# Optimization experiments

Hardware: AMD Instinct MI355X
Metric: run time of the kernel (lower is better)

Reference implementation:

```python
import jax, jax.numpy as jnp
import numpy as np

B = 100_000   # graph nodes in batch
C = 1_000     # virtual-node clusters
D = 512       # in_dim (attention hidden dim)
OUT = 512     # out_dim


def setup_inputs() -> dict:
    key = jax.random.key(0)
    ks = jax.random.split(key, 9)
    h = jax.random.normal(ks[0], (B, D), dtype=jnp.float32)
    g = jax.random.normal(ks[1], (C, D), dtype=jnp.float32)
    # vn_index[:,1] is the cluster id of node i; arange%C guarantees every
    # cluster is present, so the per-cluster concat has exactly C rows in
    # sorted-cluster-id order (matching torch .unique() iteration order).
    vn_index = jnp.stack([jnp.arange(B, dtype=jnp.int32),
                          jnp.arange(B, dtype=jnp.int32) % C], axis=1)
    n_id = jnp.arange(B, dtype=jnp.int32)
    s = 1.0 / np.sqrt(D)
    Wq = jax.random.uniform(ks[2], (D, D), jnp.float32, -s, s)   # query_proj (no bias)
    Wk = jax.random.uniform(ks[3], (D, D), jnp.float32, -s, s)   # key_proj (no bias)
    attn_bias = jax.random.uniform(ks[4], (D,), jnp.float32, -0.1, 0.1)
    Ws = jax.random.uniform(ks[5], (1, D), jnp.float32, -s, s)   # score_proj weight
    bs = jax.random.uniform(ks[6], (1,), jnp.float32, -s, s)     # score_proj bias
    so = 1.0 / np.sqrt(D)
    W = jax.random.uniform(ks[7], (OUT, D), jnp.float32, -so, so)  # final Linear
    b = jax.random.uniform(ks[8], (OUT,), jnp.float32, -so, so)
    return {"h": h, "g": g, "vn_index": vn_index, "n_id": n_id,
            "Wq": Wq, "Wk": Wk, "attn_bias": attn_bias, "Ws": Ws, "bs": bs,
            "W": W, "b": b}


def reference(h, g, vn_index, n_id, Wq, Wk, attn_bias, Ws, bs, W, b):
    # cluster id for each batch node (B,)
    cluster = vn_index[n_id, 1]
    # additive attention, vectorized over all nodes (replaces per-cluster loop)
    qp = g @ Wq.T                                   # (C, D) query proj per cluster
    kp = h @ Wk.T                                   # (B, D) key proj per node
    score = jnp.tanh(kp + qp[cluster] + attn_bias) @ Ws[0] + bs[0]  # (B,)
    # segment softmax over each cluster
    smax = jax.ops.segment_max(score, cluster, num_segments=C)      # (C,)
    e = jnp.exp(score - smax[cluster])                              # (B,)
    denom = jax.ops.segment_sum(e, cluster, num_segments=C)         # (C,)
    attn = e / denom[cluster]                                       # (B,)
    # attention-weighted sum of node features per cluster -> (C, D)
    ctx = jax.ops.segment_sum(attn[:, None] * h, cluster, num_segments=C)
    # final projection + tanh activation -> (C, OUT)
    return jnp.tanh(ctx @ W.T + b)
```

## Files before the change

kernel.cpp:

```cpp
#include <hip/hip_runtime.h>
#include <stdint.h>

#define D_DIM 512

typedef __attribute__((ext_vector_type(8))) short bf16x8;
typedef __attribute__((ext_vector_type(4))) float f32x4;
typedef __attribute__((ext_vector_type(4))) short short4_t;
typedef __attribute__((ext_vector_type(4))) float float4_t;

__device__ __forceinline__ unsigned short f2bf(float f) {
  unsigned u = __float_as_uint(f);
  u += 0x7FFFu + ((u >> 16) & 1u);
  return (unsigned short)(u >> 16);
}

__device__ __forceinline__ float bf2f(unsigned short s) {
  return __uint_as_float(((unsigned)s) << 16);
}

__device__ __forceinline__ float tanh_fast(float x) {
  float e = __expf(2.0f * x);
  return 1.0f - 2.0f / (e + 1.0f);
}

#define GLOAD_LDS16(gsrc, ldst) \
  __builtin_amdgcn_global_load_lds((const __attribute__((address_space(1))) void*)(gsrc), \
                                   (__attribute__((address_space(3))) void*)(ldst), 16, 0, 0)


__global__ void cvt_f32_bf16_k(const float* __restrict__ in, unsigned short* __restrict__ out, int n4) {
  int i = blockIdx.x * blockDim.x + threadIdx.x;
  if (i < n4) {
    float4_t v = ((const float4_t*)in)[i];
    short4_t s;
    s.x = (short)f2bf(v.x); s.y = (short)f2bf(v.y);
    s.z = (short)f2bf(v.z); s.w = (short)f2bf(v.w);
    ((short4_t*)out)[i] = s;
  }
}

__global__ void cvt3_f32_bf16_k(const float* __restrict__ a, const float* __restrict__ b,
                                const float* __restrict__ c, unsigned short* __restrict__ out,
                                int n4each) {
  int i = blockIdx.x * blockDim.x + threadIdx.x;
  if (i >= 3 * n4each) return;
  int sel = i / n4each, j = i - sel * n4each;
  const float* src = (sel == 0) ? a : (sel == 1) ? b : c;
  float4_t v = ((const float4_t*)src)[j];
  short4_t s;
  s.x = (short)f2bf(v.x); s.y = (short)f2bf(v.y);
  s.z = (short)f2bf(v.z); s.w = (short)f2bf(v.w);
  ((short4_t*)out)[i] = s;
}

__global__ void prep_cluster_k(const int* __restrict__ vn, const int* __restrict__ nid,
                               int* __restrict__ cl, int* __restrict__ counts, int B) {
  int i = blockIdx.x * blockDim.x + threadIdx.x;
  if (i < B) {
    int c = vn[2 * nid[i] + 1];
    cl[i] = c;
    atomicAdd(&counts[c], 1);
  }
}

__global__ void prefix_k(const int* __restrict__ counts, int* __restrict__ starts,
                         int* __restrict__ cursor, int C) {
  __shared__ int sh[1024];
  int t = threadIdx.x;
  int v = (t < C) ? counts[t] : 0;
  sh[t] = v;
  __syncthreads();
  for (int off = 1; off < 1024; off <<= 1) {
    int x = (t >= off) ? sh[t - off] : 0;
    __syncthreads();
    sh[t] += x;
    __syncthreads();
  }
  if (t < C) { int st = sh[t] - v; starts[t] = st; cursor[t] = st; }
  if (t == 1023) starts[C] = sh[1023];
}

__global__ void scatter_k(const int* __restrict__ cl, int* __restrict__ cursor,
                          int* __restrict__ order, int B) {
  int i = blockIdx.x * blockDim.x + threadIdx.x;
  if (i < B) {
    int pos = atomicAdd(&cursor[cl[i]], 1);
    order[pos] = i;
  }
}

__device__ __forceinline__ unsigned enc_f(float f) {
  unsigned u = __float_as_uint(f);
  return (u & 0x80000000u) ? ~u : (u | 0x80000000u);
}
__device__ __forceinline__ float dec_f(unsigned u) {
  return __uint_as_float((u & 0x80000000u) ? (u & 0x7FFFFFFFu) : ~u);
}

__global__ void seg_max_k(const float* __restrict__ score, const int* __restrict__ cl,
                          unsigned* __restrict__ smax, int B) {
  int i = blockIdx.x * blockDim.x + threadIdx.x;
  if (i < B) atomicMax(&smax[cl[i]], enc_f(score[i]));
}

__global__ void seg_expsum_k(const float* __restrict__ score, const int* __restrict__ cl,
                             const unsigned* __restrict__ smax, float* __restrict__ ev,
                             float* __restrict__ denom, int B) {
  int i = blockIdx.x * blockDim.x + threadIdx.x;
  if (i < B) {
    int c = cl[i];
    float x = __expf(score[i] - dec_f(smax[c]));
    ev[i] = x;
    atomicAdd(&denom[c], x);
  }
}

__global__ __launch_bounds__(256)
void ctx_k(const unsigned short* __restrict__ hbf, const float* __restrict__ ev,
           const int* __restrict__ order, const int* __restrict__ starts,
           const float* __restrict__ denom, float* __restrict__ ctx) {
  int c = blockIdx.x;
  int t = threadIdx.x;
  int s0 = starts[c], s1 = starts[c + 1];
  float a0 = 0.f, a1 = 0.f;
  int j = s0;
  for (; j + 3 < s1; j += 4) {
    int i0 = order[j], i1 = order[j + 1], i2 = order[j + 2], i3 = order[j + 3];
    float e0 = ev[i0], e1 = ev[i1], e2 = ev[i2], e3 = ev[i3];
    unsigned u0 = *(const unsigned*)(hbf + (size_t)i0 * D_DIM + t * 2);
    unsigned u1 = *(const unsigned*)(hbf + (size_t)i1 * D_DIM + t * 2);
    unsigned u2 = *(const unsigned*)(hbf + (size_t)i2 * D_DIM + t * 2);
    unsigned u3 = *(const unsigned*)(hbf + (size_t)i3 * D_DIM + t * 2);
    a0 += e0 * bf2f((unsigned short)u0) + e1 * bf2f((unsigned short)u1)
        + e2 * bf2f((unsigned short)u2) + e3 * bf2f((unsigned short)u3);
    a1 += e0 * bf2f((unsigned short)(u0 >> 16)) + e1 * bf2f((unsigned short)(u1 >> 16))
        + e2 * bf2f((unsigned short)(u2 >> 16)) + e3 * bf2f((unsigned short)(u3 >> 16));
  }
  for (; j < s1; ++j) {
    int i0 = order[j];
    float e0 = ev[i0];
    unsigned u0 = *(const unsigned*)(hbf + (size_t)i0 * D_DIM + t * 2);
    a0 += e0 * bf2f((unsigned short)u0);
    a1 += e0 * bf2f((unsigned short)(u0 >> 16));
  }
  float inv = 1.0f / denom[c];
  float2 r = make_float2(a0 * inv, a1 * inv);
  *(float2*)(&ctx[(size_t)c * D_DIM + t * 2]) = r;
}

__global__ __launch_bounds__(1024)
void gemm256sq_score_k(const unsigned short* __restrict__ Abf,
                       const unsigned short* __restrict__ Bw, int M,
                       const float* __restrict__ qb, const int* __restrict__ cl,
                       const float* __restrict__ Ws, float* __restrict__ out)
{
  __shared__ unsigned short AB[2][16384];
  __shared__ float red[256][4];
  __shared__ int clds[256];

  const int t = threadIdx.x;
  const int lane = t & 63;
  const int w = t >> 6;
  const int wr = w >> 2, wc = w & 3;
  const int l15 = lane & 15, l4 = lane >> 4;

  int id;
  {
    int nwg = gridDim.x;
    int q = nwg >> 3, r = nwg & 7;
    int xcd = blockIdx.x & 7, pos = blockIdx.x >> 3;
    id = (xcd < r ? xcd * (q + 1) : r * (q + 1) + (xcd - r) * q) + pos;
  }
  const int n0 = (id & 1) * 256;
  const int m0 = (id >> 1) * 256;

  const int rin = lane >> 2;
  const int lrow = w * 16 + rin;
  const int sslot = (lane & 3) ^ ((lrow >> 1) & 3);
  int rowA = m0 + lrow; if (rowA > M - 1) rowA = M - 1;
  const unsigned short* srcA = Abf + (size_t)rowA * 512 + sslot * 8;
  const unsigned short* srcB = Bw + (size_t)(n0 + lrow) * 512 + sslot * 8;

  int offA[4], offB[4];
  #pragma unroll
  for (int mi = 0; mi < 4; ++mi) {
    int row = wr * 64 + mi * 16 + l15;
    offA[mi] = row * 64 + ((l4 ^ ((row >> 1) & 3)) * 16);
  }
  #pragma unroll
  for (int ni = 0; ni < 4; ++ni) {
    int row = wc * 64 + ni * 16 + l15;
    offB[ni] = 16384 + row * 64 + ((l4 ^ ((row >> 1) & 3)) * 16);
  }

  f32x4 acc[4][4];
  #pragma unroll
  for (int mi = 0; mi < 4; ++mi)
    #pragma unroll
    for (int ni = 0; ni < 4; ++ni)
      acc[mi][ni] = (f32x4){0.f, 0.f, 0.f, 0.f};

  GLOAD_LDS16(srcA, ((char*)&AB[0][0]) + w * 1024);
  GLOAD_LDS16(srcB, ((char*)&AB[0][8192]) + w * 1024);
  __builtin_amdgcn_sched_barrier(0);

  #pragma unroll
  for (int kt = 0; kt < 16; ++kt) {
    const int b = kt & 1;
    asm volatile("s_waitcnt vmcnt(0)" ::: "memory");
    __builtin_amdgcn_sched_barrier(0);
    __builtin_amdgcn_s_barrier();
    __builtin_amdgcn_sched_barrier(0);

    if (kt < 15) {
      const int k1 = (kt + 1) * 32;
      GLOAD_LDS16(srcA + k1, ((char*)&AB[b ^ 1][0]) + w * 1024);
      GLOAD_LDS16(srcB + k1, ((char*)&AB[b ^ 1][8192]) + w * 1024);
    }

    bf16x8 a[4], bv[4];
    #pragma unroll
    for (int mi = 0; mi < 4; ++mi)
      a[mi] = *(const bf16x8*)(((const char*)AB[b]) + offA[mi]);
    #pragma unroll
    for (int ni = 0; ni < 4; ++ni)
      bv[ni] = *(const bf16x8*)(((const char*)AB[b]) + offB[ni]);
    __builtin_amdgcn_s_setprio(1);
    #pragma unroll
    for (int mi = 0; mi < 4; ++mi)
      #pragma unroll
      for (int ni = 0; ni < 4; ++ni)
        acc[mi][ni] = __builtin_amdgcn_mfma_f32_16x16x32_bf16(a[mi], bv[ni], acc[mi][ni], 0, 0, 0);
    __builtin_amdgcn_s_setprio(0);
    __builtin_amdgcn_sched_barrier(0);
  }

  if (t < 256) {
    int gm = m0 + t;
    clds[t] = cl[gm < M ? gm : M - 1];
  }
  __syncthreads();
  #pragma unroll
  for (int mi = 0; mi < 4; ++mi) {
    #pragma unroll
    for (int r = 0; r < 4; ++r) {
      int rowt = wr * 64 + mi * 16 + l4 * 4 + r;
      int c = clds[rowt];
      const float* qrow = &qb[(size_t)c * 512];
      float s = 0.f;
      #pragma unroll
      for (int ni = 0; ni < 4; ++ni) {
        int gcol = n0 + wc * 64 + ni * 16 + l15;
        float x = acc[mi][ni][r] + qrow[gcol];
        s += tanh_fast(x) * Ws[gcol];
      }
      s += __shfl_xor(s, 1);
      s += __shfl_xor(s, 2);
      s += __shfl_xor(s, 4);
      s += __shfl_xor(s, 8);
      if (l15 == 0) red[rowt][wc] = s;
    }
  }
  __syncthreads();
  if (t < 256) {
    int gm = m0 + t;
    if (gm < M) atomicAdd(&out[gm], red[t][0] + red[t][1] + red[t][2] + red[t][3]);
  }
}

template<int EPI>
__global__ __launch_bounds__(256)
void gemm128_k(const unsigned short* __restrict__ Abf,
               const unsigned short* __restrict__ Bw, int M,
               const float* __restrict__ bias, float* __restrict__ out)
{
  __shared__ unsigned short As[2][128 * 32];
  __shared__ unsigned short Bs[2][128 * 32];

  const int t = threadIdx.x;
  const int lane = t & 63;
  const int w = t >> 6;
  const int wr = w >> 1, wc = w & 1;
  const int l15 = lane & 15, l4 = lane >> 4;

  const int nwg = gridDim.x;
  int id = blockIdx.x;
  if ((nwg & 7) == 0) id = (id & 7) * (nwg >> 3) + (id >> 3);
  const int n0 = (id & 3) * 128;
  const int m0 = (id >> 2) * 128;

  const int rin = lane >> 2;
  const int sl = lane & 3;

  const unsigned short* srcA[2];
  const unsigned short* srcB[2];
  int dstOff[2];
  #pragma unroll
  for (int c = 0; c < 2; ++c) {
    int chunk = w * 2 + c;
    int row = chunk * 16 + rin;
    int slot = sl ^ ((row >> 1) & 3);
    int ga = m0 + row; if (ga > M - 1) ga = M - 1;
    srcA[c] = Abf + (size_t)ga * 512 + slot * 8;
    srcB[c] = Bw + (size_t)(n0 + row) * 512 + slot * 8;
    dstOff[c] = chunk * 1024;
  }

  int offA[4], offB[4];
  #pragma unroll
  for (int mi = 0; mi < 4; ++mi) {
    int row = wr * 64 + mi * 16 + l15;
    offA[mi] = row * 64 + ((l4 ^ ((row >> 1) & 3)) * 16);
  }
  #pragma unroll
  for (int ni = 0; ni < 4; ++ni) {
    int row = wc * 64 + ni * 16 + l15;
    offB[ni] = row * 64 + ((l4 ^ ((row >> 1) & 3)) * 16);
  }

  f32x4 acc[4][4];
  #pragma unroll
  for (int mi = 0; mi < 4; ++mi)
    #pragma unroll
    for (int ni = 0; ni < 4; ++ni)
      acc[mi][ni] = (f32x4){0.f, 0.f, 0.f, 0.f};

  #pragma unroll
  for (int c = 0; c < 2; ++c) {
    GLOAD_LDS16(srcA[c], ((char*)As[0]) + dstOff[c]);
    GLOAD_LDS16(srcB[c], ((char*)Bs[0]) + dstOff[c]);
  }
  __builtin_amdgcn_sched_barrier(0);

  #pragma unroll
  for (int it = 0; it < 16; ++it) {
    const int cur = it & 1;
    asm volatile("s_waitcnt vmcnt(0)" ::: "memory");
    __builtin_amdgcn_sched_barrier(0);
    __builtin_amdgcn_s_barrier();
    __builtin_amdgcn_sched_barrier(0);
    if (it < 15) {
      const int k1 = (it + 1) * 32;
      #pragma unroll
      for (int c = 0; c < 2; ++c) {
        GLOAD_LDS16(srcA[c] + k1, ((char*)As[cur ^ 1]) + dstOff[c]);
        GLOAD_LDS16(srcB[c] + k1, ((char*)Bs[cur ^ 1]) + dstOff[c]);
      }
    }
    {
      bf16x8 af[4], bfv[4];
      #pragma unroll
      for (int mi = 0; mi < 4; ++mi)
        af[mi] = *(const bf16x8*)(((const char*)As[cur]) + offA[mi]);
      #pragma unroll
      for (int ni = 0; ni < 4; ++ni)
        bfv[ni] = *(const bf16x8*)(((const char*)Bs[cur]) + offB[ni]);
      #pragma unroll
      for (int mi = 0; mi < 4; ++mi)
        #pragma unroll
        for (int ni = 0; ni < 4; ++ni)
          acc[mi][ni] = __builtin_amdgcn_mfma_f32_16x16x32_bf16(af[mi], bfv[ni], acc[mi][ni], 0, 0, 0);
    }
    __builtin_amdgcn_sched_barrier(0);
  }

  #pragma unroll
  for (int mi = 0; mi < 4; ++mi) {
    #pragma unroll
    for (int r = 0; r < 4; ++r) {
      int gm = m0 + wr * 64 + mi * 16 + l4 * 4 + r;
      if (gm < M) {
        #pragma unroll
        for (int ni = 0; ni < 4; ++ni) {
          int gcol = n0 + wc * 64 + ni * 16 + l15;
          float v = acc[mi][ni][r] + bias[gcol];
          if (EPI == 2) v = tanh_fast(v);
          out[(size_t)gm * 512 + gcol] = v;
        }
      }
    }
  }
}


extern "C" void kernel_launch(void* const* d_in, const int* in_sizes, int n_in,
                              void* d_out, int out_size, void* d_ws, size_t ws_size,
                              hipStream_t stream) {
  const float* h  = (const float*)d_in[0];
  const float* g  = (const float*)d_in[1];
  const int*   vn = (const int*)d_in[2];
  const int*   nid= (const int*)d_in[3];
  const float* Wq = (const float*)d_in[4];
  const float* Wk = (const float*)d_in[5];
  const float* ab = (const float*)d_in[6];
  const float* Ws = (const float*)d_in[7];
  const float* W  = (const float*)d_in[9];
  const float* b  = (const float*)d_in[10];

  const int B = in_sizes[3];
  const int C = in_sizes[1] / D_DIM;

  char* wsb = (char*)d_ws;
  size_t off = 0;
  auto alloc = [&](size_t bytes) -> void* {
    void* p = wsb + off;
    off += (bytes + 255) & ~(size_t)255;
    return p;
  };

  unsigned short* hbf   = (unsigned short*)alloc((size_t)B * 512 * 2);
  unsigned short* gbf   = (unsigned short*)alloc((size_t)C * 512 * 2);
  unsigned short* ctxbf = (unsigned short*)alloc((size_t)C * 512 * 2);
  unsigned short* Wk_bf = (unsigned short*)alloc((size_t)512 * 512 * 2);
  unsigned short* Wq_bf = (unsigned short*)alloc((size_t)512 * 512 * 2);
  unsigned short* W_bf  = (unsigned short*)alloc((size_t)512 * 512 * 2);
  float* qb    = (float*)alloc((size_t)C * 512 * 4);
  float* ctx   = (float*)alloc((size_t)C * 512 * 4);
  float* score = (float*)alloc((size_t)B * 4);
  float* ev    = (float*)alloc((size_t)B * 4);
  int*   cl    = (int*)alloc((size_t)B * 4);
  int*   order = (int*)alloc((size_t)B * 4);
  int*      counts = (int*)alloc((size_t)C * 4);
  unsigned* smax   = (unsigned*)alloc((size_t)C * 4);
  float*    denom  = (float*)alloc((size_t)C * 4);
  int* starts = (int*)alloc((size_t)(C + 1) * 4);
  int* cursor = (int*)alloc((size_t)C * 4);
  (void)ws_size; (void)n_in; (void)out_size;

  size_t zlen = (size_t)((char*)denom - (char*)counts) + (size_t)C * 4;
  hipMemsetAsync(counts, 0, zlen, stream);
  hipMemsetAsync(score, 0, (size_t)B * 4, stream);

  cvt_f32_bf16_k<<<(B * 512 / 4 + 255) / 256, 256, 0, stream>>>(h, hbf, B * 512 / 4);
  cvt_f32_bf16_k<<<(C * 512 / 4 + 255) / 256, 256, 0, stream>>>(g, gbf, C * 512 / 4);
  const int n4w = 512 * 512 / 4;
  cvt3_f32_bf16_k<<<(3 * n4w + 255) / 256, 256, 0, stream>>>(Wk, Wq, W, Wk_bf, n4w);

  prep_cluster_k<<<(B + 255) / 256, 256, 0, stream>>>(vn, nid, cl, counts, B);
  prefix_k<<<1, 1024, 0, stream>>>(counts, starts, cursor, C);
  scatter_k<<<(B + 255) / 256, 256, 0, stream>>>(cl, cursor, order, B);

  gemm128_k<0><<<4 * ((C + 127) / 128), 256, 0, stream>>>(gbf, Wq_bf, C, ab, qb);

  gemm256sq_score_k<<<2 * ((B + 255) / 256), 1024, 0, stream>>>(
      hbf, Wk_bf, B, qb, cl, Ws, score);

  seg_max_k<<<(B + 255) / 256, 256, 0, stream>>>(score, cl, smax, B);
  seg_expsum_k<<<(B + 255) / 256, 256, 0, stream>>>(score, cl, smax, ev, denom, B);
  ctx_k<<<C, 256, 0, stream>>>(hbf, ev, order, starts, denom, ctx);

  cvt_f32_bf16_k<<<(C * 512 / 4 + 255) / 256, 256, 0, stream>>>(ctx, ctxbf, C * 512 / 4);

  gemm128_k<2><<<4 * ((C + 127) / 128), 256, 0, stream>>>(ctxbf, W_bf, C, b, (float*)d_out);
}
```

Before: 242.6 us.

## Restructure score GEMM to 512 threads with triple-buffered LDS and phased MFMA

The fused key-projection/score GEMM moves from 16 waves with 4x4 MFMA tiles per wave to 8 waves with 8x4 tiles per wave. Its LDS staging goes from double to triple buffering, prefetching two K-steps ahead with partial vmcnt waits. Each K-step is split into four phases that interleave global-to-LDS loads with MFMA groups, separated by barriers. The goal is to hide global load latency and give each wave more MFMA work per LDS read, at the cost of more registers, 96KB of LDS per block and extra barriers per K-step.

```diff
diff --git a/kernel.cpp b/kernel.cpp
--- a/kernel.cpp
+++ b/kernel.cpp
@@ -148,13 +148,13 @@
   *(float2*)(&ctx[(size_t)c * D_DIM + t * 2]) = r;
 }
 
-__global__ __launch_bounds__(1024)
-void gemm256sq_score_k(const unsigned short* __restrict__ Abf,
-                       const unsigned short* __restrict__ Bw, int M,
-                       const float* __restrict__ qb, const int* __restrict__ cl,
-                       const float* __restrict__ Ws, float* __restrict__ out)
+__global__ __launch_bounds__(512, 2)
+void gemm256_phase_score_k(const unsigned short* __restrict__ Abf,
+                           const unsigned short* __restrict__ Bw, int M,
+                           const float* __restrict__ qb, const int* __restrict__ cl,
+                           const float* __restrict__ Ws, float* __restrict__ out)
 {
-  __shared__ unsigned short AB[2][16384];
+  __shared__ char ABmem[98304];
   __shared__ float red[256][4];
   __shared__ int clds[256];
 
@@ -174,65 +174,97 @@
   const int n0 = (id & 1) * 256;
   const int m0 = (id >> 1) * 256;
 
-  const int rin = lane >> 2;
-  const int lrow = w * 16 + rin;
-  const int sslot = (lane & 3) ^ ((lrow >> 1) & 3);
-  int rowA = m0 + lrow; if (rowA > M - 1) rowA = M - 1;
-  const unsigned short* srcA = Abf + (size_t)rowA * 512 + sslot * 8;
-  const unsigned short* srcB = Bw + (size_t)(n0 + lrow) * 512 + sslot * 8;
-
-  int offA[4], offB[4];
-  #pragma unroll
-  for (int mi = 0; mi < 4; ++mi) {
-    int row = wr * 64 + mi * 16 + l15;
+  const unsigned short* srcA[2];
+  const unsigned short* srcB[2];
+  #pragma unroll
+  for (int i = 0; i < 2; ++i) {
+    int row = i * 128 + w * 16 + (lane >> 2);
+    int ss = (lane & 3) ^ ((row >> 1) & 3);
+    int ga = m0 + row; if (ga > M - 1) ga = M - 1;
+    srcA[i] = Abf + (size_t)ga * 512 + ss * 8;
+    srcB[i] = Bw + (size_t)(n0 + row) * 512 + ss * 8;
+  }
+  const int dstOff = w * 1024;
+
+  int offA[8], offB[4];
+  #pragma unroll
+  for (int mi = 0; mi < 8; ++mi) {
+    int row = wr * 128 + mi * 16 + l15;
     offA[mi] = row * 64 + ((l4 ^ ((row >> 1) & 3)) * 16);
   }
   #pragma unroll
   for (int ni = 0; ni < 4; ++ni) {
     int row = wc * 64 + ni * 16 + l15;
-    offB[ni] = 16384 + row * 64 + ((l4 ^ ((row >> 1) & 3)) * 16);
-  }
-
-  f32x4 acc[4][4];
-  #pragma unroll
-  for (int mi = 0; mi < 4; ++mi)
+    offB[ni] = row * 64 + ((l4 ^ ((row >> 1) & 3)) * 16);
+  }
+
+  f32x4 acc[8][4];
+  #pragma unroll
+  for (int mi = 0; mi < 8; ++mi)
     #pragma unroll
     for (int ni = 0; ni < 4; ++ni)
       acc[mi][ni] = (f32x4){0.f, 0.f, 0.f, 0.f};
 
-  GLOAD_LDS16(srcA, ((char*)&AB[0][0]) + w * 1024);
-  GLOAD_LDS16(srcB, ((char*)&AB[0][8192]) + w * 1024);
+  #pragma unroll
+  for (int i = 0; i < 2; ++i) {
+    GLOAD_LDS16(srcA[i], ABmem + 0 * 16384 + i * 8192 + dstOff);
+    GLOAD_LDS16(srcB[i], ABmem + 49152 + 0 * 16384 + i * 8192 + dstOff);
+  }
   __builtin_amdgcn_sched_barrier(0);
+  #pragma unroll
+  for (int i = 0; i < 2; ++i) {
+    GLOAD_LDS16(srcA[i] + 32, ABmem + 1 * 16384 + i * 8192 + dstOff);
+    GLOAD_LDS16(srcB[i] + 32, ABmem + 49152 + 1 * 16384 + i * 8192 + dstOff);
+  }
+  __builtin_amdgcn_sched_barrier(0);
 
   #pragma unroll
   for (int kt = 0; kt < 16; ++kt) {
-    const int b = kt & 1;
-    asm volatile("s_waitcnt vmcnt(0)" ::: "memory");
+    const int st = kt % 3;
+    const char* Aslot = ABmem + st * 16384;
+    const char* Bslot = ABmem + 49152 + st * 16384;
+    char* AslotN = ABmem + ((kt + 2) % 3) * 16384;
+    char* BslotN = ABmem + 49152 + ((kt + 2) % 3) * 16384;
+
+    if (kt < 14) asm volatile("s_waitcnt vmcnt(4)" ::: "memory");
+    else         asm volatile("s_waitcnt vmcnt(0)" ::: "memory");
     __builtin_amdgcn_sched_barrier(0);
     __builtin_amdgcn_s_barrier();
     __builtin_amdgcn_sched_barrier(0);
 
-    if (kt < 15) {
-      const int k1 = (kt + 1) * 32;
-      GLOAD_LDS16(srcA + k1, ((char*)&AB[b ^ 1][0]) + w * 1024);
-      GLOAD_LDS16(srcB + k1, ((char*)&AB[b ^ 1][8192]) + w * 1024);
+    bf16x8 bfr[4];
+    #pragma unroll
+    for (int p = 0; p < 4; ++p) {
+      bf16x8 alo, ahi;
+      if (p == 0) {
+        #pragma unroll
+        for (int ni = 0; ni < 4; ++ni)
+          bfr[ni] = *(const bf16x8*)(Bslot + offB[ni]);
+      }
+      alo = *(const bf16x8*)(Aslot + offA[2 * p]);
+      ahi = *(const bf16x8*)(Aslot + offA[2 * p + 1]);
+
+      if (kt < 14) {
+        const int ka = (kt + 2) * 32;
+        if (p < 2) GLOAD_LDS16(srcA[p] + ka, AslotN + p * 8192 + dstOff);
+        else       GLOAD_LDS16(srcB[p - 2] + ka, BslotN + (p - 2) * 8192 + dstOff);
+      }
+      __builtin_amdgcn_sched_barrier(0);
+      __builtin_amdgcn_s_barrier();
+      asm volatile("s_waitcnt lgkmcnt(0)" ::: "memory");
+      __builtin_amdgcn_sched_barrier(0);
+
+      __builtin_amdgcn_s_setprio(1);
+      #pragma unroll
+      for (int ni = 0; ni < 4; ++ni) {
+        acc[2 * p][ni]     = __builtin_amdgcn_mfma_f32_16x16x32_bf16(alo, bfr[ni], acc[2 * p][ni], 0, 0, 0);
+        acc[2 * p + 1][ni] = __builtin_amdgcn_mfma_f32_16x16x32_bf16(ahi, bfr[ni], acc[2 * p + 1][ni], 0, 0, 0);
+      }
+      __builtin_amdgcn_s_setprio(0);
+      __builtin_amdgcn_sched_barrier(0);
+      __builtin_amdgcn_s_barrier();
+      __builtin_amdgcn_sched_barrier(0);
     }
-
-    bf16x8 a[4], bv[4];
-    #pragma unroll
-    for (int mi = 0; mi < 4; ++mi)
-      a[mi] = *(const bf16x8*)(((const char*)AB[b]) + offA[mi]);
-    #pragma unroll
-    for (int ni = 0; ni < 4; ++ni)
-      bv[ni] = *(const bf16x8*)(((const char*)AB[b]) + offB[ni]);
-    __builtin_amdgcn_s_setprio(1);
-    #pragma unroll
-    for (int mi = 0; mi < 4; ++mi)
-      #pragma unroll
-      for (int ni = 0; ni < 4; ++ni)
-        acc[mi][ni] = __builtin_amdgcn_mfma_f32_16x16x32_bf16(a[mi], bv[ni], acc[mi][ni], 0, 0, 0);
-    __builtin_amdgcn_s_setprio(0);
-    __builtin_amdgcn_sched_barrier(0);
   }
 
   if (t < 256) {
@@ -241,10 +273,10 @@
   }
   __syncthreads();
   #pragma unroll
-  for (int mi = 0; mi < 4; ++mi) {
+  for (int mi = 0; mi < 8; ++mi) {
     #pragma unroll
     for (int r = 0; r < 4; ++r) {
-      int rowt = wr * 64 + mi * 16 + l4 * 4 + r;
+      int rowt = wr * 128 + mi * 16 + l4 * 4 + r;
       int c = clds[rowt];
       const float* qrow = &qb[(size_t)c * 512];
       float s = 0.f;
@@ -442,7 +474,7 @@
 
   gemm128_k<0><<<4 * ((C + 127) / 128), 256, 0, stream>>>(gbf, Wq_bf, C, ab, qb);
 
-  gemm256sq_score_k<<<2 * ((B + 255) / 256), 1024, 0, stream>>>(
+  gemm256_phase_score_k<<<2 * ((B + 255) / 256), 512, 0, stream>>>(
       hbf, Wk_bf, B, qb, cl, Ws, score);
 
   seg_max_k<<<(B + 255) / 256, 256, 0, stream>>>(score, cl, smax, B);
```

Measured after the change: 274.1 us. 13.0% more time.
